# Optimization experiments

Measured on AMD Instinct MI355X. Metric: run time of the kernel, lower is better.

The kernel has to match this reference:

```python
import jax, jax.numpy as jnp
import numpy as np

T, N, E, F_IN, C = 8, 50000, 800000, 64, 64


def setup_inputs() -> dict:
    key = jax.random.key(0)
    ks = jax.random.split(key, 32)
    inp = {
        "x": jax.random.normal(ks[0], (T, N, F_IN), dtype=jnp.float32),
        "edge_index": jax.random.randint(ks[1], (2, E), 0, N, dtype=jnp.int32),
        "edge_weight": jax.random.uniform(ks[2], (E,), dtype=jnp.float32),
    }
    s = 0.05
    names = ["xz", "hz", "xr", "hr", "xh", "hh"]
    for i, nm in enumerate(names):
        cin = F_IN if nm[0] == "x" else C
        inp[f"W{nm}0"] = jax.random.normal(ks[3 + 3 * i], (cin, C), dtype=jnp.float32) * s
        inp[f"W{nm}1"] = jax.random.normal(ks[4 + 3 * i], (cin, C), dtype=jnp.float32) * s
        inp[f"b{nm}"] = jax.random.normal(ks[5 + 3 * i], (C,), dtype=jnp.float32) * s
    inp["W_lin"] = jax.random.normal(ks[30], (C, 1), dtype=jnp.float32) * s
    inp["b_lin"] = jax.random.normal(ks[31], (1,), dtype=jnp.float32) * s
    return inp


def reference(x, edge_index, edge_weight,
              Wxz0, Wxz1, bxz, Whz0, Whz1, bhz,
              Wxr0, Wxr1, bxr, Whr0, Whr1, bhr,
              Wxh0, Wxh1, bxh, Whh0, Whh1, bhh,
              W_lin, b_lin):
    src, dst = edge_index[0], edge_index[1]
    n = x.shape[1]
    # sym-normalized L_hat = -D^{-1/2} A D^{-1/2} (ChebConv, lambda_max=2)
    deg = jnp.zeros((n,), x.dtype).at[src].add(edge_weight)
    dinv = jnp.where(deg > 0, jax.lax.rsqrt(jnp.maximum(deg, 1e-12)), 0.0)
    nw = -edge_weight * dinv[src] * dinv[dst]  # (E,)

    def cheb(v, W0, W1, b):
        # K=2 Chebyshev: v @ W0 + (L_hat v) @ W1 + b ; v: (T, N, Cin)
        msgs = nw[None, :, None] * v[:, src, :]          # (T, E, Cin)
        tx1 = jnp.zeros_like(v).at[:, dst, :].add(msgs)  # scatter-add over nodes
        return v @ W0 + tx1 @ W1 + b

    H = jnp.zeros(x.shape[:2] + (Whz0.shape[0],), x.dtype)  # H=None -> zeros
    Z = jax.nn.sigmoid(cheb(x, Wxz0, Wxz1, bxz) + cheb(H, Whz0, Whz1, bhz))
    R = jax.nn.sigmoid(cheb(x, Wxr0, Wxr1, bxr) + cheb(H, Whr0, Whr1, bhr))
    Ht = jnp.tanh(cheb(x, Wxh0, Wxh1, bxh) + cheb(R * H, Whh0, Whh1, bhh))
    H = Z * H + (1.0 - Z) * Ht
    h = jax.nn.relu(H)
    return h @ W_lin + b_lin
```

## Files before the change

kernel.cpp:

```cpp
#include <hip/hip_runtime.h>

#define T_ 8
#define N_ 50000
#define E_ 800000
#define C_ 64
#define OVF_CAP 131072

typedef __attribute__((ext_vector_type(8))) short bf16x8;
typedef __attribute__((ext_vector_type(4))) float f32x4;

__device__ inline short f2bf(float f) {
    union { float f; unsigned int u; } v; v.f = f;
    unsigned int u = v.u + 0x7FFFu + ((v.u >> 16) & 1u);
    return (short)(u >> 16);
}
__device__ inline float bf2f_lo(unsigned int u) {
    union { unsigned int u; float f; } v; v.u = u << 16;
    return v.f;
}
__device__ inline float bf2f_hi(unsigned int u) {
    union { unsigned int u; float f; } v; v.u = u & 0xffff0000u;
    return v.f;
}

__global__ __launch_bounds__(256) void hist_kernel(const int* __restrict__ src,
                                                   const float* __restrict__ w,
                                                   float* __restrict__ degw) {
    int e = blockIdx.x * 256 + threadIdx.x;
    atomicAdd(&degw[src[e]], w[e]);
}

__global__ __launch_bounds__(256) void fused_prep_kernel(
        const int* __restrict__ src, const int* __restrict__ dst,
        const float* __restrict__ w, const float* __restrict__ degw,
        int* __restrict__ cnt,
        int2* __restrict__ es, int cap,
        int* __restrict__ ovfcnt, int4* __restrict__ ovf,
        const float* __restrict__ x, unsigned short* __restrict__ xb,
        const float* __restrict__ Wz0, const float* __restrict__ Wz1,
        const float* __restrict__ Wh0, const float* __restrict__ Wh1,
        short* __restrict__ swz) {
    if (blockIdx.x < 3125) {
        int e = blockIdx.x * 256 + threadIdx.x;
        int s = src[e], d = dst[e];
        float ds = degw[s], dd = degw[d];
        float is = ds > 0.f ? rsqrtf(fmaxf(ds, 1e-12f)) : 0.f;
        float idv = dd > 0.f ? rsqrtf(fmaxf(dd, 1e-12f)) : 0.f;
        float nwv = -w[e] * is * idv;
        int pos = atomicAdd(&cnt[d], 1);
        if (pos < cap) {
            es[d * cap + pos] = make_int2(s, __float_as_int(nwv));
        } else {
            int op = atomicAdd(ovfcnt, 1);
            if (op < OVF_CAP) ovf[op] = make_int4(d, s, __float_as_int(nwv), 0);
        }
    } else if (blockIdx.x < 15625) {
        int id = (blockIdx.x - 3125) * 256 + threadIdx.x;
        int c8 = id & 7;
        int t = (id >> 3) & 7;
        int n = id >> 6;
        const float* xr = x + ((long long)t * N_ + n) * C_ + c8 * 8;
        float4 a = *(const float4*)(xr);
        float4 b = *(const float4*)(xr + 4);
        bf16x8 o;
        o[0] = f2bf(a.x); o[1] = f2bf(a.y); o[2] = f2bf(a.z); o[3] = f2bf(a.w);
        o[4] = f2bf(b.x); o[5] = f2bf(b.y); o[6] = f2bf(b.z); o[7] = f2bf(b.w);
        *(bf16x8*)(xb + (long long)id * 8) = o;
    } else {
        int idx = (blockIdx.x - 15625) * 256 + threadIdx.x;
        int j = idx & 7;
        int lane = (idx >> 3) & 63;
        int kb = (idx >> 9) & 1;
        int c = (idx >> 10) & 3;
        int mat = idx >> 12;
        const float* W = (mat == 0) ? Wz0 : (mat == 1) ? Wz1 : (mat == 2) ? Wh0 : Wh1;
        int k = kb * 32 + (lane >> 4) * 8 + j;
        int n = c * 16 + (lane & 15);
        swz[idx] = f2bf(W[k * 64 + n]);
    }
}

#define ACC8(W, V)                                                       \
    acc[0] += (W) * bf2f_lo((V).x); acc[1] += (W) * bf2f_hi((V).x);      \
    acc[2] += (W) * bf2f_lo((V).y); acc[3] += (W) * bf2f_hi((V).y);      \
    acc[4] += (W) * bf2f_lo((V).z); acc[5] += (W) * bf2f_hi((V).z);      \
    acc[6] += (W) * bf2f_lo((V).w); acc[7] += (W) * bf2f_hi((V).w);

__global__ __launch_bounds__(256) void gather_node_kernel(
        const int* __restrict__ cnt, const int2* __restrict__ es, int cap,
        const int* __restrict__ ovfcnt, const int4* __restrict__ ovf,
        const unsigned short* __restrict__ xb, const short* __restrict__ swz,
        const float* __restrict__ bxz, const float* __restrict__ bhz,
        const float* __restrict__ bxh, const float* __restrict__ bhh,
        const float* __restrict__ Wlin, const float* __restrict__ blin,
        float* __restrict__ out) {
    __shared__ unsigned short ltx[32 * 72];
    __shared__ float laz[2][16][65];

    int lane = threadIdx.x & 63;
    int wid = threadIdx.x >> 6;
    int base = blockIdx.x * 4;

    {
        int d = base + wid;
        int t = lane >> 3;
        int oct = lane & 7;
        int2 pk = (lane < cap) ? es[d * cap + lane] : make_int2(0, 0);
        int m = cnt[d];
        int mb = m < cap ? m : cap;

        float acc[8] = {0.f, 0.f, 0.f, 0.f, 0.f, 0.f, 0.f, 0.f};
        const unsigned short* xbase = xb + lane * 8;
        int k = 0;
        for (; k + 3 < mb; k += 4) {
            int s0 = __shfl(pk.x, k);
            int s1 = __shfl(pk.x, k + 1);
            int s2 = __shfl(pk.x, k + 2);
            int s3 = __shfl(pk.x, k + 3);
            uint4 v0 = *(const uint4*)(xbase + (long long)s0 * 512);
            uint4 v1 = *(const uint4*)(xbase + (long long)s1 * 512);
            uint4 v2 = *(const uint4*)(xbase + (long long)s2 * 512);
            uint4 v3 = *(const uint4*)(xbase + (long long)s3 * 512);
            float w0 = __int_as_float(__shfl(pk.y, k));
            float w1 = __int_as_float(__shfl(pk.y, k + 1));
            float w2 = __int_as_float(__shfl(pk.y, k + 2));
            float w3 = __int_as_float(__shfl(pk.y, k + 3));
            ACC8(w0, v0);
            ACC8(w1, v1);
            ACC8(w2, v2);
            ACC8(w3, v3);
        }
        for (; k < mb; ++k) {
            int s0 = __shfl(pk.x, k);
            float w0 = __int_as_float(__shfl(pk.y, k));
            uint4 v0 = *(const uint4*)(xbase + (long long)s0 * 512);
            ACC8(w0, v0);
        }
        if (m > cap) {
            int oc = *ovfcnt;
            if (oc > OVF_CAP) oc = OVF_CAP;
            for (int i = 0; i < oc; ++i) {
                int4 o = ovf[i];
                if (o.x == d) {
                    float w0 = __int_as_float(o.z);
                    uint4 v0 = *(const uint4*)(xbase + (long long)o.y * 512);
                    ACC8(w0, v0);
                }
            }
        }
        uint4 ob;
        ob.x = (unsigned int)(unsigned short)f2bf(acc[0]) |
               ((unsigned int)(unsigned short)f2bf(acc[1]) << 16);
        ob.y = (unsigned int)(unsigned short)f2bf(acc[2]) |
               ((unsigned int)(unsigned short)f2bf(acc[3]) << 16);
        ob.z = (unsigned int)(unsigned short)f2bf(acc[4]) |
               ((unsigned int)(unsigned short)f2bf(acc[5]) << 16);
        ob.w = (unsigned int)(unsigned short)f2bf(acc[6]) |
               ((unsigned int)(unsigned short)f2bf(acc[7]) << 16);
        int r = wid * 8 + t;
        *(uint4*)(ltx + r * 72 + oct * 8) = ob;
    }
    __syncthreads();

    int mt = wid >> 1;
    int g = wid & 1;
    int c16 = lane & 15;
    int kq = lane >> 4;
    int r_blk = mt * 16 + c16;
    const unsigned short* xr = xb + (long long)(base * 8 + r_blk) * C_ + kq * 8;
    bf16x8 ax0 = *(const bf16x8*)(xr);
    bf16x8 ax1 = *(const bf16x8*)(xr + 32);
    bf16x8 at0 = *(const bf16x8*)(ltx + r_blk * 72 + kq * 8);
    bf16x8 at1 = *(const bf16x8*)(ltx + r_blk * 72 + 32 + kq * 8);

    const float* bA = g ? bxh : bxz;
    const float* bB = g ? bhh : bhz;
    const short* wA = swz + (2 * g) * 4096 + lane * 8;
    const short* wB = swz + (2 * g + 1) * 4096 + lane * 8;

    f32x4 a4[4];
#pragma unroll
    for (int c = 0; c < 4; ++c) {
        int col = c * 16 + c16;
        float bv = bA[col] + bB[col];
        a4[c] = (f32x4){bv, bv, bv, bv};
    }
#pragma unroll
    for (int c = 0; c < 4; ++c) {
        bf16x8 bA0 = *(const bf16x8*)(wA + (c * 2 + 0) * 512);
        bf16x8 bA1 = *(const bf16x8*)(wA + (c * 2 + 1) * 512);
        bf16x8 bB0 = *(const bf16x8*)(wB + (c * 2 + 0) * 512);
        bf16x8 bB1 = *(const bf16x8*)(wB + (c * 2 + 1) * 512);
        a4[c] = __builtin_amdgcn_mfma_f32_16x16x32_bf16(ax0, bA0, a4[c], 0, 0, 0);
        a4[c] = __builtin_amdgcn_mfma_f32_16x16x32_bf16(ax1, bA1, a4[c], 0, 0, 0);
        a4[c] = __builtin_amdgcn_mfma_f32_16x16x32_bf16(at0, bB0, a4[c], 0, 0, 0);
        a4[c] = __builtin_amdgcn_mfma_f32_16x16x32_bf16(at1, bB1, a4[c], 0, 0, 0);
    }

    if (g == 0) {
#pragma unroll
        for (int c = 0; c < 4; ++c)
#pragma unroll
            for (int r = 0; r < 4; ++r)
                laz[mt][kq * 4 + r][c * 16 + c16] = a4[c][r];
    }
    __syncthreads();
    if (g == 1) {
        float part[4] = {0.f, 0.f, 0.f, 0.f};
#pragma unroll
        for (int c = 0; c < 4; ++c) {
            int col = c * 16 + c16;
            float wl = Wlin[col];
#pragma unroll
            for (int r = 0; r < 4; ++r) {
                float a = laz[mt][kq * 4 + r][col];
                float b = a4[c][r];
                float z = 1.f / (1.f + __expf(-a));
                float aa = fabsf(b);
                float e = __expf(-2.f * aa);
                float ht = copysignf((1.f - e) / (1.f + e), b);
                float h = fmaxf((1.f - z) * ht, 0.f);
                part[r] += h * wl;
            }
        }
#pragma unroll
        for (int m = 1; m <= 8; m <<= 1) {
#pragma unroll
            for (int r = 0; r < 4; ++r) part[r] += __shfl_xor(part[r], m);
        }
        if (c16 == 0) {
            float bl = blin[0];
#pragma unroll
            for (int r = 0; r < 4; ++r) {
                int rb = mt * 16 + kq * 4 + r;
                out[(long long)(rb & 7) * N_ + base + (rb >> 3)] = part[r] + bl;
            }
        }
    }
}

extern "C" void kernel_launch(void* const* d_in, const int* in_sizes, int n_in,
                              void* d_out, int out_size, void* d_ws, size_t ws_size,
                              hipStream_t stream) {
    const float* x    = (const float*)d_in[0];
    const int*   ei   = (const int*)d_in[1];
    const float* w    = (const float*)d_in[2];
    const float* Wxz0 = (const float*)d_in[3];
    const float* Wxz1 = (const float*)d_in[4];
    const float* bxz  = (const float*)d_in[5];
    const float* bhz  = (const float*)d_in[8];
    const float* Wxh0 = (const float*)d_in[15];
    const float* Wxh1 = (const float*)d_in[16];
    const float* bxh  = (const float*)d_in[17];
    const float* bhh  = (const float*)d_in[20];
    const float* Wlin = (const float*)d_in[21];
    const float* blin = (const float*)d_in[22];
    float* out = (float*)d_out;

    const int* src = ei;
    const int* dst = ei + E_;

    char* ws = (char*)d_ws;
    size_t off = 0;
    auto alloc = [&](size_t bytes) {
        char* p = ws + off;
        off = (off + bytes + 511) & ~(size_t)511;
        return p;
    };
    short* swz         = (short*)alloc(4 * 4096 * sizeof(short));
    float* degw        = (float*)alloc((size_t)N_ * 4);
    int*   cnt         = (int*)alloc((size_t)N_ * 4);
    int*   ovfcnt      = (int*)alloc(512);
    int4*  ovf         = (int4*)alloc((size_t)OVF_CAP * 16);
    unsigned short* xb = (unsigned short*)alloc((size_t)T_ * N_ * C_ * 2);
    size_t fixed = off;

    int cap = 16;
    for (int c : {64, 48, 32, 24}) {
        if (fixed + (size_t)N_ * c * 8 + 512 <= ws_size) { cap = c; break; }
    }
    int2* es = (int2*)alloc((size_t)N_ * cap * 8);

    hipMemsetAsync(degw, 0, (size_t)N_ * 4, stream);
    hipMemsetAsync(cnt, 0, (size_t)N_ * 4, stream);
    hipMemsetAsync(ovfcnt, 0, 4, stream);

    hist_kernel<<<3125, 256, 0, stream>>>(src, w, degw);

    fused_prep_kernel<<<15689, 256, 0, stream>>>(src, dst, w, degw, cnt,
                                                 es, cap, ovfcnt, ovf,
                                                 x, xb, Wxz0, Wxz1, Wxh0, Wxh1, swz);

    gather_node_kernel<<<N_ / 4, 256, 0, stream>>>(
        cnt, es, cap, ovfcnt, ovf, xb, swz,
        bxz, bhz, bxh, bhh, Wlin, blin, out);
}
```

Before: 407.5 us.

## Pad degree/count atomics and split x conversion across both prep kernels

Spaces the per-node degree and count atomic targets 16 elements apart so each node sits on its own 64-byte segment, which is meant to reduce same-line atomic contention. Half of the x-to-bf16 conversion moves into the histogram kernel, so the bandwidth-heavy work overlaps with the latency-bound atomics in both prep kernels. The cost is larger memsets (about 6.4 MB instead of 400 KB) and scattered, less cache-friendly reads of degw and cnt.

```diff
diff --git a/kernel.cpp b/kernel.cpp
--- a/kernel.cpp
+++ b/kernel.cpp
@@ -5,6 +5,7 @@
 #define E_ 800000
 #define C_ 64
 #define OVF_CAP 131072
+#define PAD 16
 
 typedef __attribute__((ext_vector_type(8))) short bf16x8;
 typedef __attribute__((ext_vector_type(4))) float f32x4;
@@ -23,14 +24,34 @@
     return v.f;
 }
 
-__global__ __launch_bounds__(256) void hist_kernel(const int* __restrict__ src,
-                                                   const float* __restrict__ w,
-                                                   float* __restrict__ degw) {
-    int e = blockIdx.x * 256 + threadIdx.x;
-    atomicAdd(&degw[src[e]], w[e]);
-}
-
-__global__ __launch_bounds__(256) void fused_prep_kernel(
+__device__ inline void xcvt_step(int id, const float* __restrict__ x,
+                                 unsigned short* __restrict__ xb) {
+    int c8 = id & 7;
+    int t = (id >> 3) & 7;
+    int n = id >> 6;
+    const float* xr = x + ((long long)t * N_ + n) * C_ + c8 * 8;
+    float4 a = *(const float4*)(xr);
+    float4 b = *(const float4*)(xr + 4);
+    bf16x8 o;
+    o[0] = f2bf(a.x); o[1] = f2bf(a.y); o[2] = f2bf(a.z); o[3] = f2bf(a.w);
+    o[4] = f2bf(b.x); o[5] = f2bf(b.y); o[6] = f2bf(b.z); o[7] = f2bf(b.w);
+    *(bf16x8*)(xb + (long long)id * 8) = o;
+}
+
+__global__ __launch_bounds__(256) void prep_a_kernel(
+        const int* __restrict__ src, const float* __restrict__ w,
+        float* __restrict__ degw,
+        const float* __restrict__ x, unsigned short* __restrict__ xb) {
+    if (blockIdx.x < 3125) {
+        int e = blockIdx.x * 256 + threadIdx.x;
+        atomicAdd(&degw[(long long)src[e] * PAD], w[e]);
+    } else {
+        int id = (blockIdx.x - 3125) * 256 + threadIdx.x;
+        xcvt_step(id, x, xb);
+    }
+}
+
+__global__ __launch_bounds__(256) void prep_b_kernel(
         const int* __restrict__ src, const int* __restrict__ dst,
         const float* __restrict__ w, const float* __restrict__ degw,
         int* __restrict__ cnt,
@@ -43,31 +64,22 @@
     if (blockIdx.x < 3125) {
         int e = blockIdx.x * 256 + threadIdx.x;
         int s = src[e], d = dst[e];
-        float ds = degw[s], dd = degw[d];
+        float ds = degw[(long long)s * PAD], dd = degw[(long long)d * PAD];
         float is = ds > 0.f ? rsqrtf(fmaxf(ds, 1e-12f)) : 0.f;
         float idv = dd > 0.f ? rsqrtf(fmaxf(dd, 1e-12f)) : 0.f;
         float nwv = -w[e] * is * idv;
-        int pos = atomicAdd(&cnt[d], 1);
+        int pos = atomicAdd(&cnt[(long long)d * PAD], 1);
         if (pos < cap) {
             es[d * cap + pos] = make_int2(s, __float_as_int(nwv));
         } else {
             int op = atomicAdd(ovfcnt, 1);
             if (op < OVF_CAP) ovf[op] = make_int4(d, s, __float_as_int(nwv), 0);
         }
-    } else if (blockIdx.x < 15625) {
-        int id = (blockIdx.x - 3125) * 256 + threadIdx.x;
-        int c8 = id & 7;
-        int t = (id >> 3) & 7;
-        int n = id >> 6;
-        const float* xr = x + ((long long)t * N_ + n) * C_ + c8 * 8;
-        float4 a = *(const float4*)(xr);
-        float4 b = *(const float4*)(xr + 4);
-        bf16x8 o;
-        o[0] = f2bf(a.x); o[1] = f2bf(a.y); o[2] = f2bf(a.z); o[3] = f2bf(a.w);
-        o[4] = f2bf(b.x); o[5] = f2bf(b.y); o[6] = f2bf(b.z); o[7] = f2bf(b.w);
-        *(bf16x8*)(xb + (long long)id * 8) = o;
+    } else if (blockIdx.x < 9375) {
+        int id = 1600000 + (blockIdx.x - 3125) * 256 + threadIdx.x;
+        xcvt_step(id, x, xb);
     } else {
-        int idx = (blockIdx.x - 15625) * 256 + threadIdx.x;
+        int idx = (blockIdx.x - 9375) * 256 + threadIdx.x;
         int j = idx & 7;
         int lane = (idx >> 3) & 63;
         int kb = (idx >> 9) & 1;
@@ -106,7 +118,7 @@
         int t = lane >> 3;
         int oct = lane & 7;
         int2 pk = (lane < cap) ? es[d * cap + lane] : make_int2(0, 0);
-        int m = cnt[d];
+        int m = cnt[(long long)d * PAD];
         int mb = m < cap ? m : cap;
 
         float acc[8] = {0.f, 0.f, 0.f, 0.f, 0.f, 0.f, 0.f, 0.f};
@@ -268,8 +280,8 @@
         return p;
     };
     short* swz         = (short*)alloc(4 * 4096 * sizeof(short));
-    float* degw        = (float*)alloc((size_t)N_ * 4);
-    int*   cnt         = (int*)alloc((size_t)N_ * 4);
+    float* degw        = (float*)alloc((size_t)N_ * PAD * 4);
+    int*   cnt         = (int*)alloc((size_t)N_ * PAD * 4);
     int*   ovfcnt      = (int*)alloc(512);
     int4*  ovf         = (int4*)alloc((size_t)OVF_CAP * 16);
     unsigned short* xb = (unsigned short*)alloc((size_t)T_ * N_ * C_ * 2);
@@ -281,15 +293,15 @@
     }
     int2* es = (int2*)alloc((size_t)N_ * cap * 8);
 
-    hipMemsetAsync(degw, 0, (size_t)N_ * 4, stream);
-    hipMemsetAsync(cnt, 0, (size_t)N_ * 4, stream);
+    hipMemsetAsync(degw, 0, (size_t)N_ * PAD * 4, stream);
+    hipMemsetAsync(cnt, 0, (size_t)N_ * PAD * 4, stream);
     hipMemsetAsync(ovfcnt, 0, 4, stream);
 
-    hist_kernel<<<3125, 256, 0, stream>>>(src, w, degw);
-
-    fused_prep_kernel<<<15689, 256, 0, stream>>>(src, dst, w, degw, cnt,
-                                                 es, cap, ovfcnt, ovf,
-                                                 x, xb, Wxz0, Wxz1, Wxh0, Wxh1, swz);
+    prep_a_kernel<<<9375, 256, 0, stream>>>(src, w, degw, x, xb);
+
+    prep_b_kernel<<<9439, 256, 0, stream>>>(src, dst, w, degw, cnt,
+                                            es, cap, ovfcnt, ovf,
+                                            x, xb, Wxz0, Wxz1, Wxh0, Wxh1, swz);
 
     gather_node_kernel<<<N_ / 4, 256, 0, stream>>>(
         cnt, es, cap, ovfcnt, ovf, xb, swz,
```

Result: faster. 397.7 us (-2.4%).

## Replace global atomic edge bucketing with two-level radix partition and shared-memory atomics

Applied to the files above, without the earlier changes.

Swaps the global-atomic degree histogram and per-destination slot allocation for a counting-sort scheme. Edges are first binned into 256-node buckets by source and by destination, using a per-block histogram, a two-kernel prefix scan and a scatter into a record array. Per-bucket kernels then compute degrees and build the per-node edge lists with shared-memory atomics only. This removes contended global atomics and random global writes, at the cost of four extra launches and an extra 12.8MB record array pass. Scatter and esbuild each use one block per 3125 edges or per 256 nodes, which is only 196 to 256 blocks and may leave much of the GPU idle.

```diff
diff --git a/kernel.cpp b/kernel.cpp
--- a/kernel.cpp
+++ b/kernel.cpp
@@ -5,6 +5,11 @@
 #define E_ 800000
 #define C_ 64
 #define OVF_CAP 131072
+#define NB 196
+#define NBLK 256
+#define EPB 3125
+#define SCN (2 * NB * NBLK)
+#define SCAN_TILES 49
 
 typedef __attribute__((ext_vector_type(8))) short bf16x8;
 typedef __attribute__((ext_vector_type(4))) float f32x4;
@@ -23,51 +28,46 @@
     return v.f;
 }
 
-__global__ __launch_bounds__(256) void hist_kernel(const int* __restrict__ src,
-                                                   const float* __restrict__ w,
-                                                   float* __restrict__ degw) {
-    int e = blockIdx.x * 256 + threadIdx.x;
-    atomicAdd(&degw[src[e]], w[e]);
-}
-
-__global__ __launch_bounds__(256) void fused_prep_kernel(
+__device__ inline void xcvt_step(int id, const float* __restrict__ x,
+                                 unsigned short* __restrict__ xb) {
+    int c8 = id & 7;
+    int t = (id >> 3) & 7;
+    int n = id >> 6;
+    const float* xr = x + ((long long)t * N_ + n) * C_ + c8 * 8;
+    float4 a = *(const float4*)(xr);
+    float4 b = *(const float4*)(xr + 4);
+    bf16x8 o;
+    o[0] = f2bf(a.x); o[1] = f2bf(a.y); o[2] = f2bf(a.z); o[3] = f2bf(a.w);
+    o[4] = f2bf(b.x); o[5] = f2bf(b.y); o[6] = f2bf(b.z); o[7] = f2bf(b.w);
+    *(bf16x8*)(xb + (long long)id * 8) = o;
+}
+
+__global__ __launch_bounds__(256) void prep_kernel(
         const int* __restrict__ src, const int* __restrict__ dst,
-        const float* __restrict__ w, const float* __restrict__ degw,
-        int* __restrict__ cnt,
-        int2* __restrict__ es, int cap,
-        int* __restrict__ ovfcnt, int4* __restrict__ ovf,
+        int* __restrict__ counts,
         const float* __restrict__ x, unsigned short* __restrict__ xb,
         const float* __restrict__ Wz0, const float* __restrict__ Wz1,
         const float* __restrict__ Wh0, const float* __restrict__ Wh1,
         short* __restrict__ swz) {
-    if (blockIdx.x < 3125) {
-        int e = blockIdx.x * 256 + threadIdx.x;
-        int s = src[e], d = dst[e];
-        float ds = degw[s], dd = degw[d];
-        float is = ds > 0.f ? rsqrtf(fmaxf(ds, 1e-12f)) : 0.f;
-        float idv = dd > 0.f ? rsqrtf(fmaxf(dd, 1e-12f)) : 0.f;
-        float nwv = -w[e] * is * idv;
-        int pos = atomicAdd(&cnt[d], 1);
-        if (pos < cap) {
-            es[d * cap + pos] = make_int2(s, __float_as_int(nwv));
-        } else {
-            int op = atomicAdd(ovfcnt, 1);
-            if (op < OVF_CAP) ovf[op] = make_int4(d, s, __float_as_int(nwv), 0);
-        }
-    } else if (blockIdx.x < 15625) {
-        int id = (blockIdx.x - 3125) * 256 + threadIdx.x;
-        int c8 = id & 7;
-        int t = (id >> 3) & 7;
-        int n = id >> 6;
-        const float* xr = x + ((long long)t * N_ + n) * C_ + c8 * 8;
-        float4 a = *(const float4*)(xr);
-        float4 b = *(const float4*)(xr + 4);
-        bf16x8 o;
-        o[0] = f2bf(a.x); o[1] = f2bf(a.y); o[2] = f2bf(a.z); o[3] = f2bf(a.w);
-        o[4] = f2bf(b.x); o[5] = f2bf(b.y); o[6] = f2bf(b.z); o[7] = f2bf(b.w);
-        *(bf16x8*)(xb + (long long)id * 8) = o;
+    if (blockIdx.x < NBLK) {
+        __shared__ int h[2 * NB];
+        int t = threadIdx.x;
+        for (int i = t; i < 2 * NB; i += 256) h[i] = 0;
+        __syncthreads();
+        int e0 = blockIdx.x * EPB;
+        for (int j = t; j < EPB; j += 256) {
+            int e = e0 + j;
+            atomicAdd(&h[src[e] >> 8], 1);
+            atomicAdd(&h[NB + (dst[e] >> 8)], 1);
+        }
+        __syncthreads();
+        for (int i = t; i < 2 * NB; i += 256)
+            counts[i * NBLK + blockIdx.x] = h[i];
+    } else if (blockIdx.x < NBLK + 12500) {
+        int id = (blockIdx.x - NBLK) * 256 + threadIdx.x;
+        xcvt_step(id, x, xb);
     } else {
-        int idx = (blockIdx.x - 15625) * 256 + threadIdx.x;
+        int idx = (blockIdx.x - NBLK - 12500) * 256 + threadIdx.x;
         int j = idx & 7;
         int lane = (idx >> 3) & 63;
         int kb = (idx >> 9) & 1;
@@ -78,6 +78,133 @@
         int n = c * 16 + (lane & 15);
         swz[idx] = f2bf(W[k * 64 + n]);
     }
+}
+
+__global__ __launch_bounds__(1024) void scan_a_kernel(int* __restrict__ cnts,
+                                                      int* __restrict__ tsum) {
+    __shared__ int wsum[16];
+    int tid = threadIdx.x, lane = tid & 63, wid = tid >> 6;
+    int i0 = blockIdx.x * 2048 + tid * 2;
+    int v0 = cnts[i0], v1 = cnts[i0 + 1];
+    int orig = v0 + v1;
+    int v = orig;
+#pragma unroll
+    for (int off = 1; off < 64; off <<= 1) {
+        int u = __shfl_up(v, off);
+        if (lane >= off) v += u;
+    }
+    if (lane == 63) wsum[wid] = v;
+    __syncthreads();
+    if (wid == 0) {
+        int s = (lane < 16) ? wsum[lane] : 0;
+#pragma unroll
+        for (int off = 1; off < 16; off <<= 1) {
+            int u = __shfl_up(s, off);
+            if (lane >= off) s += u;
+        }
+        if (lane < 16) wsum[lane] = s;
+    }
+    __syncthreads();
+    int wpre = wid ? wsum[wid - 1] : 0;
+    int ex = wpre + v - orig;
+    cnts[i0] = ex;
+    cnts[i0 + 1] = ex + v0;
+    if (tid == 0) tsum[blockIdx.x] = wsum[15];
+}
+
+__global__ __launch_bounds__(1024) void scan_b_kernel(const int* __restrict__ tsum,
+                                                      int* __restrict__ cnts) {
+    __shared__ int soff[SCAN_TILES];
+    int tid = threadIdx.x, lane = tid & 63, wid = tid >> 6;
+    if (wid == 0) {
+        int own = (lane < SCAN_TILES) ? tsum[lane] : 0;
+        int s = own;
+#pragma unroll
+        for (int off = 1; off < 64; off <<= 1) {
+            int u = __shfl_up(s, off);
+            if (lane >= off) s += u;
+        }
+        if (lane < SCAN_TILES) soff[lane] = s - own;
+    }
+    __syncthreads();
+    int off = soff[blockIdx.x];
+    int i0 = blockIdx.x * 2048 + tid;
+    cnts[i0] += off;
+    cnts[i0 + 1024] += off;
+}
+
+__global__ __launch_bounds__(256) void scatter_kernel(
+        const int* __restrict__ src, const int* __restrict__ dst,
+        const float* __restrict__ w, const int* __restrict__ scn,
+        int2* __restrict__ rec) {
+    __shared__ int offs[2 * NB];
+    int t = threadIdx.x;
+    for (int i = t; i < 2 * NB; i += 256)
+        offs[i] = scn[i * NBLK + blockIdx.x];
+    __syncthreads();
+    int e0 = blockIdx.x * EPB;
+    for (int j = t; j < EPB; j += 256) {
+        int e = e0 + j;
+        int s = src[e], d = dst[e];
+        float wv = w[e];
+        int r0 = atomicAdd(&offs[s >> 8], 1);
+        rec[r0] = make_int2(s, __float_as_int(wv));
+        int r1 = atomicAdd(&offs[NB + (d >> 8)], 1);
+        rec[r1] = make_int2(s | ((d & 255) << 16), __float_as_int(wv));
+    }
+}
+
+__global__ __launch_bounds__(256) void degw_kernel(
+        const int2* __restrict__ rec, const int* __restrict__ scn,
+        float* __restrict__ degw) {
+    __shared__ float acc[256];
+    int t = threadIdx.x, b = blockIdx.x;
+    acc[t] = 0.f;
+    __syncthreads();
+    int s0 = scn[b * NBLK];
+    int s1 = (b == NB - 1) ? E_ : scn[(b + 1) * NBLK];
+    for (int j = s0 + t; j < s1; j += 256) {
+        int2 r = rec[j];
+        atomicAdd(&acc[r.x & 255], __int_as_float(r.y));
+    }
+    __syncthreads();
+    int node = b * 256 + t;
+    if (node < N_) degw[node] = acc[t];
+}
+
+__global__ __launch_bounds__(256) void esbuild_kernel(
+        const int2* __restrict__ rec, const int* __restrict__ scn,
+        const float* __restrict__ degw, int* __restrict__ cnt,
+        int2* __restrict__ es, int cap,
+        int* __restrict__ ovfcnt, int4* __restrict__ ovf) {
+    __shared__ int cl[256];
+    __shared__ float di[256];
+    int t = threadIdx.x, b = blockIdx.x;
+    cl[t] = 0;
+    int node = b * 256 + t;
+    float dd = (node < N_) ? degw[node] : 0.f;
+    di[t] = dd > 0.f ? rsqrtf(fmaxf(dd, 1e-12f)) : 0.f;
+    __syncthreads();
+    int s0 = scn[(NB + b) * NBLK];
+    int s1 = (b == NB - 1) ? 2 * E_ : scn[(NB + b + 1) * NBLK];
+    for (int j = s0 + t; j < s1; j += 256) {
+        int2 r = rec[j];
+        int s = r.x & 0xffff;
+        int dl = (r.x >> 16) & 255;
+        float ds = degw[s];
+        float is = ds > 0.f ? rsqrtf(fmaxf(ds, 1e-12f)) : 0.f;
+        float nwv = -__int_as_float(r.y) * is * di[dl];
+        int rank = atomicAdd(&cl[dl], 1);
+        int d = b * 256 + dl;
+        if (rank < cap) {
+            es[d * cap + rank] = make_int2(s, __float_as_int(nwv));
+        } else {
+            int op = atomicAdd(ovfcnt, 1);
+            if (op < OVF_CAP) ovf[op] = make_int4(d, s, __float_as_int(nwv), 0);
+        }
+    }
+    __syncthreads();
+    if (node < N_) cnt[node] = cl[t];
 }
 
 #define ACC8(W, V)                                                       \
@@ -272,6 +399,9 @@
     int*   cnt         = (int*)alloc((size_t)N_ * 4);
     int*   ovfcnt      = (int*)alloc(512);
     int4*  ovf         = (int4*)alloc((size_t)OVF_CAP * 16);
+    int*   counts      = (int*)alloc((size_t)SCN * 4);
+    int*   tsum        = (int*)alloc((size_t)SCAN_TILES * 4);
+    int2*  rec         = (int2*)alloc((size_t)2 * E_ * 8);
     unsigned short* xb = (unsigned short*)alloc((size_t)T_ * N_ * C_ * 2);
     size_t fixed = off;
 
@@ -281,15 +411,20 @@
     }
     int2* es = (int2*)alloc((size_t)N_ * cap * 8);
 
-    hipMemsetAsync(degw, 0, (size_t)N_ * 4, stream);
-    hipMemsetAsync(cnt, 0, (size_t)N_ * 4, stream);
     hipMemsetAsync(ovfcnt, 0, 4, stream);
 
-    hist_kernel<<<3125, 256, 0, stream>>>(src, w, degw);
-
-    fused_prep_kernel<<<15689, 256, 0, stream>>>(src, dst, w, degw, cnt,
-                                                 es, cap, ovfcnt, ovf,
-                                                 x, xb, Wxz0, Wxz1, Wxh0, Wxh1, swz);
+    prep_kernel<<<NBLK + 12500 + 64, 256, 0, stream>>>(
+        src, dst, counts, x, xb, Wxz0, Wxz1, Wxh0, Wxh1, swz);
+
+    scan_a_kernel<<<SCAN_TILES, 1024, 0, stream>>>(counts, tsum);
+    scan_b_kernel<<<SCAN_TILES, 1024, 0, stream>>>(tsum, counts);
+
+    scatter_kernel<<<NBLK, 256, 0, stream>>>(src, dst, w, counts, rec);
+
+    degw_kernel<<<NB, 256, 0, stream>>>(rec, counts, degw);
+
+    esbuild_kernel<<<NB, 256, 0, stream>>>(rec, counts, degw, cnt,
+                                           es, cap, ovfcnt, ovf);
 
     gather_node_kernel<<<N_ / 4, 256, 0, stream>>>(
         cnt, es, cap, ovfcnt, ovf, xb, swz,
```

After: 368.1 us. 9.7% less time.

## Replace atomic CSR build with cooperative bucketed counting-sort prep kernel

Applied to the files above, without the earlier changes.

Replaces the separate degree histogram, memsets and global-atomic CSR fill with one cooperative kernel. It bucket-sorts edges by source and destination block through a two-level prefix scan, computes degrees with shared-memory atomics, and writes per-node edge slots with LDS-local ranks. The x-to-bf16 conversion and weight swizzle run inside the same kernel. This removes heavy global atomic contention and launch overhead, at the cost of several grid syncs, extra passes over an intermediate record buffer of two records per edge, and more workspace.

```diff
diff --git a/kernel.cpp b/kernel.cpp
--- a/kernel.cpp
+++ b/kernel.cpp
@@ -1,10 +1,19 @@
 #include <hip/hip_runtime.h>
+#include <hip/hip_cooperative_groups.h>
+
+namespace cg = cooperative_groups;
 
 #define T_ 8
 #define N_ 50000
 #define E_ 800000
 #define C_ 64
 #define OVF_CAP 131072
+#define NB 196
+#define NBLK 256
+#define EPB 3125
+#define SCN (2 * NB * NBLK)
+#define XCVT_UNITS 12500
+#define WPREP_UNITS 64
 
 typedef __attribute__((ext_vector_type(8))) short bf16x8;
 typedef __attribute__((ext_vector_type(4))) float f32x4;
@@ -23,60 +32,190 @@
     return v.f;
 }
 
-__global__ __launch_bounds__(256) void hist_kernel(const int* __restrict__ src,
-                                                   const float* __restrict__ w,
-                                                   float* __restrict__ degw) {
-    int e = blockIdx.x * 256 + threadIdx.x;
-    atomicAdd(&degw[src[e]], w[e]);
-}
-
-__global__ __launch_bounds__(256) void fused_prep_kernel(
-        const int* __restrict__ src, const int* __restrict__ dst,
-        const float* __restrict__ w, const float* __restrict__ degw,
-        int* __restrict__ cnt,
-        int2* __restrict__ es, int cap,
-        int* __restrict__ ovfcnt, int4* __restrict__ ovf,
-        const float* __restrict__ x, unsigned short* __restrict__ xb,
-        const float* __restrict__ Wz0, const float* __restrict__ Wz1,
-        const float* __restrict__ Wh0, const float* __restrict__ Wh1,
-        short* __restrict__ swz) {
-    if (blockIdx.x < 3125) {
-        int e = blockIdx.x * 256 + threadIdx.x;
-        int s = src[e], d = dst[e];
-        float ds = degw[s], dd = degw[d];
-        float is = ds > 0.f ? rsqrtf(fmaxf(ds, 1e-12f)) : 0.f;
-        float idv = dd > 0.f ? rsqrtf(fmaxf(dd, 1e-12f)) : 0.f;
-        float nwv = -w[e] * is * idv;
-        int pos = atomicAdd(&cnt[d], 1);
-        if (pos < cap) {
-            es[d * cap + pos] = make_int2(s, __float_as_int(nwv));
+__device__ inline void xcvt_step(int id, const float* __restrict__ x,
+                                 unsigned short* __restrict__ xb) {
+    int c8 = id & 7;
+    int t = (id >> 3) & 7;
+    int n = id >> 6;
+    const float* xr = x + ((long long)t * N_ + n) * C_ + c8 * 8;
+    float4 a = *(const float4*)(xr);
+    float4 b = *(const float4*)(xr + 4);
+    bf16x8 o;
+    o[0] = f2bf(a.x); o[1] = f2bf(a.y); o[2] = f2bf(a.z); o[3] = f2bf(a.w);
+    o[4] = f2bf(b.x); o[5] = f2bf(b.y); o[6] = f2bf(b.z); o[7] = f2bf(b.w);
+    *(bf16x8*)(xb + (long long)id * 8) = o;
+}
+
+struct CoopParams {
+    const int* src; const int* dst; const float* w;
+    const float* x;
+    const float* Wz0; const float* Wz1; const float* Wh0; const float* Wh1;
+    int* counts; int* tsum; int* soff;
+    int2* rec;
+    float* degw; int* cnt;
+    int2* es; int cap;
+    int* ovfcnt; int4* ovf;
+    unsigned short* xb; short* swz;
+};
+
+__global__ __launch_bounds__(256, 8) void coop_prep_kernel(CoopParams p) {
+    cg::grid_group grid = cg::this_grid();
+    int tid = threadIdx.x;
+    int bid = blockIdx.x;
+    int G = gridDim.x;
+
+    __shared__ int h[2 * NB];
+    __shared__ int sc[520];
+    __shared__ float facc[256];
+    __shared__ int cl[256];
+    __shared__ float di[256];
+
+    if (bid == 0 && tid == 0) *p.ovfcnt = 0;
+    for (int c = bid; c < NBLK; c += G) {
+        for (int i = tid; i < 2 * NB; i += 256) h[i] = 0;
+        __syncthreads();
+        int e0 = c * EPB;
+        for (int j = tid; j < EPB; j += 256) {
+            int e = e0 + j;
+            atomicAdd(&h[p.src[e] >> 8], 1);
+            atomicAdd(&h[NB + (p.dst[e] >> 8)], 1);
+        }
+        __syncthreads();
+        for (int i = tid; i < 2 * NB; i += 256)
+            p.counts[i * NBLK + c] = h[i];
+        __syncthreads();
+    }
+    for (int u = bid; u < XCVT_UNITS + WPREP_UNITS; u += G) {
+        if (u < XCVT_UNITS) {
+            xcvt_step(u * 256 + tid, p.x, p.xb);
         } else {
-            int op = atomicAdd(ovfcnt, 1);
-            if (op < OVF_CAP) ovf[op] = make_int4(d, s, __float_as_int(nwv), 0);
-        }
-    } else if (blockIdx.x < 15625) {
-        int id = (blockIdx.x - 3125) * 256 + threadIdx.x;
-        int c8 = id & 7;
-        int t = (id >> 3) & 7;
-        int n = id >> 6;
-        const float* xr = x + ((long long)t * N_ + n) * C_ + c8 * 8;
-        float4 a = *(const float4*)(xr);
-        float4 b = *(const float4*)(xr + 4);
-        bf16x8 o;
-        o[0] = f2bf(a.x); o[1] = f2bf(a.y); o[2] = f2bf(a.z); o[3] = f2bf(a.w);
-        o[4] = f2bf(b.x); o[5] = f2bf(b.y); o[6] = f2bf(b.z); o[7] = f2bf(b.w);
-        *(bf16x8*)(xb + (long long)id * 8) = o;
-    } else {
-        int idx = (blockIdx.x - 15625) * 256 + threadIdx.x;
-        int j = idx & 7;
-        int lane = (idx >> 3) & 63;
-        int kb = (idx >> 9) & 1;
-        int c = (idx >> 10) & 3;
-        int mat = idx >> 12;
-        const float* W = (mat == 0) ? Wz0 : (mat == 1) ? Wz1 : (mat == 2) ? Wh0 : Wh1;
-        int k = kb * 32 + (lane >> 4) * 8 + j;
-        int n = c * 16 + (lane & 15);
-        swz[idx] = f2bf(W[k * 64 + n]);
+            int idx = (u - XCVT_UNITS) * 256 + tid;
+            int j = idx & 7;
+            int lane = (idx >> 3) & 63;
+            int kb = (idx >> 9) & 1;
+            int cc = (idx >> 10) & 3;
+            int mat = idx >> 12;
+            const float* W = (mat == 0) ? p.Wz0 : (mat == 1) ? p.Wz1
+                            : (mat == 2) ? p.Wh0 : p.Wh1;
+            int k = kb * 32 + (lane >> 4) * 8 + j;
+            int n = cc * 16 + (lane & 15);
+            p.swz[idx] = f2bf(W[k * 64 + n]);
+        }
+    }
+    grid.sync();
+
+    for (int t = bid; t < 2 * NB; t += G) {
+        int v = p.counts[t * 256 + tid];
+        int orig = v;
+        int lane = tid & 63, wv = tid >> 6;
+#pragma unroll
+        for (int off = 1; off < 64; off <<= 1) {
+            int u = __shfl_up(v, off);
+            if (lane >= off) v += u;
+        }
+        if (lane == 63) sc[wv] = v;
+        __syncthreads();
+        if (tid == 0) {
+            int s = 0;
+#pragma unroll
+            for (int i = 0; i < 4; ++i) { int x2 = sc[i]; sc[i] = s; s += x2; }
+            sc[4] = s;
+        }
+        __syncthreads();
+        p.counts[t * 256 + tid] = sc[wv] + v - orig;
+        if (tid == 0) p.tsum[t] = sc[4];
+        __syncthreads();
+    }
+    grid.sync();
+
+    if (bid == 0) {
+        int i0 = 2 * tid, i1 = 2 * tid + 1;
+        int v0 = (i0 < 2 * NB) ? p.tsum[i0] : 0;
+        int v1 = (i1 < 2 * NB) ? p.tsum[i1] : 0;
+        int pr = v0 + v1;
+        int v = pr;
+        int lane = tid & 63, wv = tid >> 6;
+#pragma unroll
+        for (int off = 1; off < 64; off <<= 1) {
+            int u = __shfl_up(v, off);
+            if (lane >= off) v += u;
+        }
+        if (lane == 63) sc[wv] = v;
+        __syncthreads();
+        if (tid == 0) {
+            int s = 0;
+#pragma unroll
+            for (int i = 0; i < 4; ++i) { int x2 = sc[i]; sc[i] = s; s += x2; }
+        }
+        __syncthreads();
+        int excl = sc[wv] + v - pr;
+        if (i0 < 2 * NB) p.soff[i0] = excl;
+        if (i1 < 2 * NB) p.soff[i1] = excl + v0;
+    }
+    grid.sync();
+
+    for (int c = bid; c < NBLK; c += G) {
+        for (int i = tid; i < 2 * NB; i += 256)
+            h[i] = p.counts[i * NBLK + c] + p.soff[i];
+        __syncthreads();
+        int e0 = c * EPB;
+        for (int j = tid; j < EPB; j += 256) {
+            int e = e0 + j;
+            int s = p.src[e], d = p.dst[e];
+            float wv = p.w[e];
+            int r0 = atomicAdd(&h[s >> 8], 1);
+            p.rec[r0] = make_int2(s, __float_as_int(wv));
+            int r1 = atomicAdd(&h[NB + (d >> 8)], 1);
+            p.rec[r1] = make_int2(s | ((d & 255) << 16), __float_as_int(wv));
+        }
+        __syncthreads();
+    }
+    grid.sync();
+
+    for (int b = bid; b < NB; b += G) {
+        facc[tid] = 0.f;
+        __syncthreads();
+        int s0 = p.counts[b * 256] + p.soff[b];
+        int s1 = (b == NB - 1) ? E_ : (p.counts[(b + 1) * 256] + p.soff[b + 1]);
+        for (int j = s0 + tid; j < s1; j += 256) {
+            int2 r = p.rec[j];
+            atomicAdd(&facc[r.x & 255], __int_as_float(r.y));
+        }
+        __syncthreads();
+        int node = b * 256 + tid;
+        if (node < N_) p.degw[node] = facc[tid];
+        __syncthreads();
+    }
+    grid.sync();
+
+    for (int b = bid; b < NB; b += G) {
+        cl[tid] = 0;
+        int node = b * 256 + tid;
+        float dd = (node < N_) ? p.degw[node] : 0.f;
+        di[tid] = dd > 0.f ? rsqrtf(fmaxf(dd, 1e-12f)) : 0.f;
+        __syncthreads();
+        int s0 = p.counts[(NB + b) * 256] + p.soff[NB + b];
+        int s1 = (b == NB - 1) ? 2 * E_
+                               : (p.counts[(NB + b + 1) * 256] + p.soff[NB + b + 1]);
+        for (int j = s0 + tid; j < s1; j += 256) {
+            int2 r = p.rec[j];
+            int s = r.x & 0xffff;
+            int dl = (r.x >> 16) & 255;
+            float ds = p.degw[s];
+            float is = ds > 0.f ? rsqrtf(fmaxf(ds, 1e-12f)) : 0.f;
+            float nwv = -__int_as_float(r.y) * is * di[dl];
+            int rank = atomicAdd(&cl[dl], 1);
+            int d = b * 256 + dl;
+            if (rank < p.cap) {
+                p.es[d * p.cap + rank] = make_int2(s, __float_as_int(nwv));
+            } else {
+                int op = atomicAdd(p.ovfcnt, 1);
+                if (op < OVF_CAP) p.ovf[op] = make_int4(d, s, __float_as_int(nwv), 0);
+            }
+        }
+        __syncthreads();
+        if (node < N_) p.cnt[node] = cl[tid];
+        __syncthreads();
     }
 }
 
@@ -219,8 +358,8 @@
                 float aa = fabsf(b);
                 float e = __expf(-2.f * aa);
                 float ht = copysignf((1.f - e) / (1.f + e), b);
-                float h = fmaxf((1.f - z) * ht, 0.f);
-                part[r] += h * wl;
+                float h2 = fmaxf((1.f - z) * ht, 0.f);
+                part[r] += h2 * wl;
             }
         }
 #pragma unroll
@@ -272,6 +411,10 @@
     int*   cnt         = (int*)alloc((size_t)N_ * 4);
     int*   ovfcnt      = (int*)alloc(512);
     int4*  ovf         = (int4*)alloc((size_t)OVF_CAP * 16);
+    int*   counts      = (int*)alloc((size_t)SCN * 4);
+    int*   tsum        = (int*)alloc((size_t)2 * NB * 4);
+    int*   soff        = (int*)alloc((size_t)2 * NB * 4);
+    int2*  rec         = (int2*)alloc((size_t)2 * E_ * 8);
     unsigned short* xb = (unsigned short*)alloc((size_t)T_ * N_ * C_ * 2);
     size_t fixed = off;
 
@@ -281,15 +424,33 @@
     }
     int2* es = (int2*)alloc((size_t)N_ * cap * 8);
 
-    hipMemsetAsync(degw, 0, (size_t)N_ * 4, stream);
-    hipMemsetAsync(cnt, 0, (size_t)N_ * 4, stream);
-    hipMemsetAsync(ovfcnt, 0, 4, stream);
-
-    hist_kernel<<<3125, 256, 0, stream>>>(src, w, degw);
-
-    fused_prep_kernel<<<15689, 256, 0, stream>>>(src, dst, w, degw, cnt,
-                                                 es, cap, ovfcnt, ovf,
-                                                 x, xb, Wxz0, Wxz1, Wxh0, Wxh1, swz);
+    static int coopGrid = 0;
+    if (coopGrid == 0) {
+        int dev = 0;
+        hipGetDevice(&dev);
+        hipDeviceProp_t prop;
+        hipGetDeviceProperties(&prop, dev);
+        int occ = 0;
+        hipOccupancyMaxActiveBlocksPerMultiprocessor(&occ, coop_prep_kernel, 256, 0);
+        if (occ < 1) occ = 1;
+        long long g = (long long)occ * prop.multiProcessorCount;
+        if (g > 2048) g = 2048;
+        if (g < 1) g = 1;
+        coopGrid = (int)g;
+    }
+
+    CoopParams p;
+    p.src = src; p.dst = dst; p.w = w; p.x = x;
+    p.Wz0 = Wxz0; p.Wz1 = Wxz1; p.Wh0 = Wxh0; p.Wh1 = Wxh1;
+    p.counts = counts; p.tsum = tsum; p.soff = soff;
+    p.rec = rec; p.degw = degw; p.cnt = cnt;
+    p.es = es; p.cap = cap;
+    p.ovfcnt = ovfcnt; p.ovf = ovf;
+    p.xb = xb; p.swz = swz;
+
+    void* args[] = {&p};
+    hipLaunchCooperativeKernel(coop_prep_kernel, dim3(coopGrid), dim3(256),
+                               args, 0, stream);
 
     gather_node_kernel<<<N_ / 4, 256, 0, stream>>>(
         cnt, es, cap, ovfcnt, ovf, xb, swz,
```

Measured after the change: 1.496 ms. 267% more time.
